# Performance work log

Hardware: AMD Instinct MI355X
Metric: run time of the kernel (lower is better)

Reference implementation:

```python
import jax, jax.numpy as jnp
import numpy as np

H = 1024      # hidden_size
NH = 16       # num_heads
DH = H // NH  # head dim
EPS = 1e-5

def layer_norm(x, g, b):
    m = jnp.mean(x, axis=-1, keepdims=True)
    v = jnp.mean(jnp.square(x - m), axis=-1, keepdims=True)
    return (x - m) * jax.lax.rsqrt(v + EPS) * g + b

def setup_inputs() -> dict:
    key = jax.random.key(0)
    ks = jax.random.split(key, 12)
    B, S = 4, 1024
    s = 0.02
    inp = {
        "x": jax.random.normal(ks[0], (B, S, H), jnp.float32),
        "attn_bias": jax.random.normal(ks[1], (B, NH, S, S), jnp.float32),
        # weights stored as (in, out): y = x @ W
        "W_Q": jax.random.normal(ks[2], (H, H), jnp.float32) * s,
        "W_K": jax.random.normal(ks[3], (H, H), jnp.float32) * s,
        "W_V": jax.random.normal(ks[4], (H, H), jnp.float32) * s,
        "W_O": jax.random.normal(ks[5], (H, H), jnp.float32) * s,
        "W_1": jax.random.normal(ks[6], (H, 4 * H), jnp.float32) * s,
        "W_2": jax.random.normal(ks[7], (H, 4 * H), jnp.float32) * s,
        "W_3": jax.random.normal(ks[8], (4 * H, H), jnp.float32) * s,
        "ln1_g": jnp.ones((H,), jnp.float32), "ln1_b": jnp.zeros((H,), jnp.float32),
        "ln2_g": jnp.ones((H,), jnp.float32), "ln2_b": jnp.zeros((H,), jnp.float32),
        "ln3_g": jnp.ones((H,), jnp.float32), "ln3_b": jnp.zeros((H,), jnp.float32),
        "ln4_g": jnp.ones((H,), jnp.float32), "ln4_b": jnp.zeros((H,), jnp.float32),
    }
    return inp

def reference(x, attn_bias, W_Q, W_K, W_V, W_O, W_1, W_2, W_3,
              ln1_g, ln1_b, ln2_g, ln2_b, ln3_g, ln3_b, ln4_g, ln4_b):
    B, S, _ = x.shape
    scale = DH ** -0.5
    # attn_in_norm
    xn = layer_norm(x, ln1_g, ln1_b)
    # biased multi-head attention
    Q = (xn @ W_Q).reshape(B, S, NH, DH)
    K = (xn @ W_K).reshape(B, S, NH, DH)
    V = (xn @ W_V).reshape(B, S, NH, DH)
    scores = jnp.einsum('bqhd,bkhd->bhqk', Q, K) * scale + attn_bias
    attn = jax.nn.softmax(scores, axis=-1)
    attn_out_prelinear = jnp.einsum('bhqk,bkhd->bqhd', attn, V).reshape(B, S, H)
    attn_out = layer_norm(attn_out_prelinear @ W_O, ln2_g, ln2_b)
    x_post_attn = x + attn_out  # dropout = identity (p=0 / eval)
    # bilinear FFN
    xn2 = layer_norm(x_post_attn, ln3_g, ln3_b)
    ff = ((xn2 @ W_1) * (xn2 @ W_2)) @ W_3
    ff_out = layer_norm(ff, ln4_g, ln4_b)
    x_post_ff = x_post_attn + ff_out
    return (x_post_attn, x_post_ff, attn_out_prelinear, ff_out)
```

## Files before the change

### kernel.cpp

```cpp
#include <hip/hip_runtime.h>
#include <math.h>

typedef unsigned short u16;
typedef unsigned int u32;
typedef __attribute__((ext_vector_type(8))) short short8v;
typedef __attribute__((ext_vector_type(4))) float f32x4;

#define H 1024
#define NH 16
#define DH 64
#define BB 4
#define SS 1024
#define MROWS (BB*SS)
#define FFD 4096
#define EPS 1e-5f
#define SCALE 0.125f

__device__ __forceinline__ u16 cvt_bf16(float v) {
  u32 u = __float_as_uint(v);
  return (u16)((u + 0x7fffu + ((u >> 16) & 1u)) >> 16);
}
__device__ __forceinline__ void split_bf16(float v, u16& h, u16& l) {
  u16 hh = cvt_bf16(v);
  float hf = __uint_as_float(((u32)hh) << 16);
  float r = v - hf;
  u16 ll = cvt_bf16(r);
  h = hh; l = ll;
}
__device__ __forceinline__ u32 pack2(u16 a, u16 b) { return (u32)a | ((u32)b << 16); }

#define GLL16(g, l) __builtin_amdgcn_global_load_lds( \
    (const __attribute__((address_space(1))) void*)(g), \
    (__attribute__((address_space(3))) void*)(l), 16, 0, 0)

#define VWAIT8 asm volatile("s_waitcnt vmcnt(8)" ::: "memory")
#define VWAIT6 asm volatile("s_waitcnt vmcnt(6)" ::: "memory")
#define VWAIT0 asm volatile("s_waitcnt vmcnt(0)" ::: "memory")
#define BAR_PRE  do { __builtin_amdgcn_s_barrier(); asm volatile("" ::: "memory"); } while (0)
#define BAR_POST do { asm volatile("" ::: "memory"); __builtin_amdgcn_s_barrier(); } while (0)

__global__ __launch_bounds__(256, 2) void gemm3_k(
    const u16* __restrict__ Ah, const u16* __restrict__ Al, int sA,
    const u16* __restrict__ B0h, const u16* __restrict__ B0l,
    const u16* __restrict__ B1h, const u16* __restrict__ B1l,
    const u16* __restrict__ B2h, const u16* __restrict__ B2l, int sB,
    float* C0, float* C1, float* C2,
    u16* E0h, u16* E0l, u16* E1h, u16* E1l, u16* EV,
    int sC, int K, int addC, int qkvmode)
{
  __shared__ u16 sAh0[4096], sAl0[4096], sBh0[4096], sBl0[4096];
  __shared__ u16 sAh1[4096], sAl1[4096], sBh1[4096], sBl1[4096];
  const int tid = threadIdx.x;
  const int wave = tid >> 6, lane = tid & 63;
  const int sel = blockIdx.x >> 3;
  const int bn = (blockIdx.x & 7) << 7;
  const int bm = blockIdx.y << 7;
  const u16* Bh = (sel == 0) ? B0h : (sel == 1) ? B1h : B2h;
  const u16* Bl = (sel == 0) ? B0l : (sel == 1) ? B1l : B2l;
  float* C = (sel == 0) ? C0 : (sel == 1) ? C1 : C2;

  const int c0 = wave, c1 = 4 + wave;
  const int row0 = c0 * 16 + (lane >> 2), row1 = c1 * 16 + (lane >> 2);
  const int sg0 = (lane & 3) ^ ((row0 >> 1) & 3);
  const int sg1 = (lane & 3) ^ ((row1 >> 1) & 3);
  const size_t offA0 = (size_t)(bm + row0) * sA + sg0 * 8;
  const size_t offA1 = (size_t)(bm + row1) * sA + sg1 * 8;
  const size_t offB0 = (size_t)(bn + row0) * sB + sg0 * 8;
  const size_t offB1 = (size_t)(bn + row1) * sB + sg1 * 8;

  const int kg = lane >> 4, r15 = lane & 15;
  const int wr = wave >> 1, wc = wave & 1;
  int aoff[4], boff[4];
  #pragma unroll
  for (int m = 0; m < 4; ++m) {
    int ra = wr * 64 + m * 16 + r15;
    aoff[m] = ra * 32 + ((kg ^ ((ra >> 1) & 3)) << 3);
    int rb = wc * 64 + m * 16 + r15;
    boff[m] = rb * 32 + ((kg ^ ((rb >> 1) & 3)) << 3);
  }

#define STAGE3(P, k0) do { \
    GLL16(Ah + offA0 + (k0), &sAh##P[c0 * 512]); \
    GLL16(Ah + offA1 + (k0), &sAh##P[c1 * 512]); \
    GLL16(Al + offA0 + (k0), &sAl##P[c0 * 512]); \
    GLL16(Al + offA1 + (k0), &sAl##P[c1 * 512]); \
    GLL16(Bh + offB0 + (k0), &sBh##P[c0 * 512]); \
    GLL16(Bh + offB1 + (k0), &sBh##P[c1 * 512]); \
    GLL16(Bl + offB0 + (k0), &sBl##P[c0 * 512]); \
    GLL16(Bl + offB1 + (k0), &sBl##P[c1 * 512]); \
  } while (0)

#define COMPUTE3(P) do { \
    short8v afh[4], afl[4], bfh[4], bfl[4]; \
    _Pragma("unroll") \
    for (int m = 0; m < 4; ++m) { \
      afh[m] = *(const short8v*)&sAh##P[aoff[m]]; \
      afl[m] = *(const short8v*)&sAl##P[aoff[m]]; \
      bfh[m] = *(const short8v*)&sBh##P[boff[m]]; \
      bfl[m] = *(const short8v*)&sBl##P[boff[m]]; \
    } \
    _Pragma("unroll") \
    for (int m = 0; m < 4; ++m) \
      _Pragma("unroll") \
      for (int n = 0; n < 4; ++n) { \
        acc[m][n] = __builtin_amdgcn_mfma_f32_16x16x32_bf16(afh[m], bfl[n], acc[m][n], 0, 0, 0); \
        acc[m][n] = __builtin_amdgcn_mfma_f32_16x16x32_bf16(afl[m], bfh[n], acc[m][n], 0, 0, 0); \
        acc[m][n] = __builtin_amdgcn_mfma_f32_16x16x32_bf16(afh[m], bfh[n], acc[m][n], 0, 0, 0); \
      } \
  } while (0)

  f32x4 acc[4][4] = {};
  STAGE3(0, 0);
  #pragma unroll 1
  for (int k0 = 0; k0 < K; k0 += 64) {
    if (k0 + 32 < K) { STAGE3(1, k0 + 32); VWAIT8; } else { VWAIT0; }
    BAR_PRE;
    COMPUTE3(0);
    BAR_POST;
    if (k0 + 64 < K) { STAGE3(0, k0 + 64); VWAIT8; } else { VWAIT0; }
    BAR_PRE;
    COMPUTE3(1);
    BAR_POST;
  }
#undef STAGE3
#undef COMPUTE3

  if (qkvmode) {
    #pragma unroll
    for (int m = 0; m < 4; ++m)
      #pragma unroll
      for (int n = 0; n < 4; ++n) {
        const int col = bn + wc * 64 + n * 16 + r15;
        const int rbase = bm + wr * 64 + m * 16 + (kg << 2);
        const int bhd = ((rbase >> 10) << 4) + (col >> 6);
        const int d = col & 63;
        const int seq0 = rbase & 1023;
        if (sel == 2) {
          ushort4 pk;
          pk.x = cvt_bf16(acc[m][n][0]); pk.y = cvt_bf16(acc[m][n][1]);
          pk.z = cvt_bf16(acc[m][n][2]); pk.w = cvt_bf16(acc[m][n][3]);
          *(ushort4*)&EV[((size_t)bhd * 64 + d) * SS + seq0] = pk;
        } else {
          u16* Th = (sel == 0) ? E0h : E1h;
          u16* Tl = (sel == 0) ? E0l : E1l;
          #pragma unroll
          for (int r = 0; r < 4; ++r) {
            u16 hh, ll; split_bf16(acc[m][n][r], hh, ll);
            const size_t idx = ((size_t)bhd * SS + seq0 + r) * DH + d;
            Th[idx] = hh; Tl[idx] = ll;
          }
        }
      }
  } else {
    #pragma unroll
    for (int m = 0; m < 4; ++m)
      #pragma unroll
      for (int n = 0; n < 4; ++n) {
        const int col = bn + wc * 64 + n * 16 + r15;
        #pragma unroll
        for (int r = 0; r < 4; ++r) {
          const int rr = bm + wr * 64 + m * 16 + (kg << 2) + r;
          const size_t idx = (size_t)rr * sC + col;
          float v = acc[m][n][r];
          if (addC) v += C[idx];
          C[idx] = v;
        }
      }
  }
}

__global__ __launch_bounds__(512, 1) void gemm_dual_k(
    const u16* __restrict__ Ah, const u16* __restrict__ Al, int sA,
    const u16* __restrict__ B1h, const u16* __restrict__ B1l,
    const u16* __restrict__ B2h, const u16* __restrict__ B2l, int sB,
    u16* __restrict__ Oh, u16* __restrict__ Ol, int sC, int K)
{
  __shared__ u16 sAh0[4096], sAl0[4096], s1h0[4096], s1l0[4096], s2h0[4096], s2l0[4096];
  __shared__ u16 sAh1[4096], sAl1[4096], s1h1[4096], s1l1[4096], s2h1[4096], s2l1[4096];
  const int tid = threadIdx.x;
  const int wave = tid >> 6, lane = tid & 63;
  const int bn = blockIdx.x << 7;
  const int bm = blockIdx.y << 7;

  const int srow = wave * 16 + (lane >> 2);
  const int sg = (lane & 3) ^ ((srow >> 1) & 3);
  const size_t offA = (size_t)(bm + srow) * sA + sg * 8;
  const size_t offB = (size_t)(bn + srow) * sB + sg * 8;

  const int kg = lane >> 4, r15 = lane & 15;
  const int wr = wave >> 2, wc = wave & 3;
  int aoff[4], boff[2];
  #pragma unroll
  for (int m = 0; m < 4; ++m) {
    int ra = wr * 64 + m * 16 + r15;
    aoff[m] = ra * 32 + ((kg ^ ((ra >> 1) & 3)) << 3);
  }
  #pragma unroll
  for (int n = 0; n < 2; ++n) {
    int rb = wc * 32 + n * 16 + r15;
    boff[n] = rb * 32 + ((kg ^ ((rb >> 1) & 3)) << 3);
  }

#define STAGED(P, k0) do { \
    GLL16(Ah  + offA + (k0), &sAh##P[wave * 512]); \
    GLL16(Al  + offA + (k0), &sAl##P[wave * 512]); \
    GLL16(B1h + offB + (k0), &s1h##P[wave * 512]); \
    GLL16(B1l + offB + (k0), &s1l##P[wave * 512]); \
    GLL16(B2h + offB + (k0), &s2h##P[wave * 512]); \
    GLL16(B2l + offB + (k0), &s2l##P[wave * 512]); \
  } while (0)

#define COMPUTED(P) do { \
    short8v afh[4], afl[4]; \
    _Pragma("unroll") \
    for (int m = 0; m < 4; ++m) { \
      afh[m] = *(const short8v*)&sAh##P[aoff[m]]; \
      afl[m] = *(const short8v*)&sAl##P[aoff[m]]; \
    } \
    _Pragma("unroll") \
    for (int n = 0; n < 2; ++n) { \
      short8v b1h = *(const short8v*)&s1h##P[boff[n]]; \
      short8v b1l = *(const short8v*)&s1l##P[boff[n]]; \
      short8v b2h = *(const short8v*)&s2h##P[boff[n]]; \
      short8v b2l = *(const short8v*)&s2l##P[boff[n]]; \
      _Pragma("unroll") \
      for (int m = 0; m < 4; ++m) { \
        acc1[m][n] = __builtin_amdgcn_mfma_f32_16x16x32_bf16(afh[m], b1l, acc1[m][n], 0, 0, 0); \
        acc1[m][n] = __builtin_amdgcn_mfma_f32_16x16x32_bf16(afl[m], b1h, acc1[m][n], 0, 0, 0); \
        acc1[m][n] = __builtin_amdgcn_mfma_f32_16x16x32_bf16(afh[m], b1h, acc1[m][n], 0, 0, 0); \
        acc2[m][n] = __builtin_amdgcn_mfma_f32_16x16x32_bf16(afh[m], b2l, acc2[m][n], 0, 0, 0); \
        acc2[m][n] = __builtin_amdgcn_mfma_f32_16x16x32_bf16(afl[m], b2h, acc2[m][n], 0, 0, 0); \
        acc2[m][n] = __builtin_amdgcn_mfma_f32_16x16x32_bf16(afh[m], b2h, acc2[m][n], 0, 0, 0); \
      } \
    } \
  } while (0)

  f32x4 acc1[4][2] = {}, acc2[4][2] = {};
  STAGED(0, 0);
  #pragma unroll 1
  for (int k0 = 0; k0 < K; k0 += 64) {
    if (k0 + 32 < K) { STAGED(1, k0 + 32); VWAIT6; } else { VWAIT0; }
    BAR_PRE;
    COMPUTED(0);
    BAR_POST;
    if (k0 + 64 < K) { STAGED(0, k0 + 64); VWAIT6; } else { VWAIT0; }
    BAR_PRE;
    COMPUTED(1);
    BAR_POST;
  }
#undef STAGED
#undef COMPUTED

  #pragma unroll
  for (int m = 0; m < 4; ++m)
    #pragma unroll
    for (int n = 0; n < 2; ++n) {
      const int col = bn + wc * 32 + n * 16 + r15;
      #pragma unroll
      for (int r = 0; r < 4; ++r) {
        const int rr = bm + wr * 64 + m * 16 + (kg << 2) + r;
        const size_t idx = (size_t)rr * sC + col;
        float p = acc1[m][n][r] * acc2[m][n][r];
        u16 hh, ll; split_bf16(p, hh, ll);
        Oh[idx] = hh; Ol[idx] = ll;
      }
    }
}

__global__ __launch_bounds__(256) void trsplit_k(const float* __restrict__ W,
    int R, int Cn, u16* __restrict__ Th, u16* __restrict__ Tl) {
  __shared__ float t[32][33];
  int n0 = blockIdx.x * 32, r0 = blockIdx.y * 32;
  int tx = threadIdx.x & 31, ty = threadIdx.x >> 5;
  #pragma unroll
  for (int i = 0; i < 4; ++i)
    t[ty + i * 8][tx] = W[(size_t)(r0 + ty + i * 8) * Cn + n0 + tx];
  __syncthreads();
  #pragma unroll
  for (int i = 0; i < 4; ++i) {
    float v = t[tx][ty + i * 8];
    u16 hh, ll; split_bf16(v, hh, ll);
    size_t o = (size_t)(n0 + ty + i * 8) * R + r0 + tx;
    Th[o] = hh; Tl[o] = ll;
  }
}

__global__ __launch_bounds__(256, 2) void attn_mfma_k(
    const u16* __restrict__ Qh, const u16* __restrict__ Ql,
    const u16* __restrict__ Kh, const u16* __restrict__ Kl,
    const u16* __restrict__ Vt, const float* __restrict__ bias,
    float* __restrict__ outp, u16* __restrict__ oph, u16* __restrict__ opl)
{
  __shared__ u16 sKh[4096], sKl[4096], sVt[4096];
  __shared__ u16 sP[5120];
  const int bh = blockIdx.y;
  const int q0 = blockIdx.x << 6;
  const int tid = threadIdx.x, w = tid >> 6, lane = tid & 63;
  const int kg = lane >> 4, r15 = lane & 15;

  short8v qfh[2], qfl[2];
  {
    const size_t qb = ((size_t)bh * SS + q0 + w * 16 + r15) * DH + kg * 8;
    qfh[0] = *(const short8v*)(Qh + qb);
    qfh[1] = *(const short8v*)(Qh + qb + 32);
    qfl[0] = *(const short8v*)(Ql + qb);
    qfl[1] = *(const short8v*)(Ql + qb + 32);
  }
  const int c0 = 2 * w, c1 = 2 * w + 1;
  const int sr0 = c0 * 8 + (lane >> 3), sr1 = c1 * 8 + (lane >> 3);
  const int sl0 = (lane & 7) ^ (sr0 & 7), sl1 = (lane & 7) ^ (sr1 & 7);
  const size_t kb0 = ((size_t)bh * SS + sr0) * DH + sl0 * 8;
  const size_t kb1 = ((size_t)bh * SS + sr1) * DH + sl1 * 8;
  const size_t vb0 = ((size_t)bh * DH + sr0) * SS + sl0 * 8;
  const size_t vb1 = ((size_t)bh * DH + sr1) * SS + sl1 * 8;
  const float* bp = bias + ((size_t)bh * SS + q0 + w * 16 + kg * 4) * SS + r15;

  float m_run[4], l_run[4];
  #pragma unroll
  for (int r = 0; r < 4; ++r) { m_run[r] = -1e30f; l_run[r] = 0.f; }
  f32x4 oacc[4] = {};

  #pragma unroll 1
  for (int t = 0; t < SS / 64; ++t) {
    const int k0 = t * 64;
    __syncthreads();
    GLL16(Kh + kb0 + (size_t)k0 * DH, &sKh[c0 * 512]);
    GLL16(Kh + kb1 + (size_t)k0 * DH, &sKh[c1 * 512]);
    GLL16(Kl + kb0 + (size_t)k0 * DH, &sKl[c0 * 512]);
    GLL16(Kl + kb1 + (size_t)k0 * DH, &sKl[c1 * 512]);
    GLL16(Vt + vb0 + k0, &sVt[c0 * 512]);
    GLL16(Vt + vb1 + k0, &sVt[c1 * 512]);
    float bv[4][4];
    #pragma unroll
    for (int r = 0; r < 4; ++r)
      #pragma unroll
      for (int nb = 0; nb < 4; ++nb)
        bv[r][nb] = bp[(size_t)r * SS + k0 + nb * 16];
    __syncthreads();

    f32x4 s[4] = {};
    #pragma unroll
    for (int nb = 0; nb < 4; ++nb) {
      const int krow = nb * 16 + r15;
      #pragma unroll
      for (int ks = 0; ks < 2; ++ks) {
        const int ch = (((ks * 4 + kg) ^ (krow & 7)) << 3);
        short8v kbh = *(const short8v*)&sKh[krow * 64 + ch];
        short8v kbl = *(const short8v*)&sKl[krow * 64 + ch];
        s[nb] = __builtin_amdgcn_mfma_f32_16x16x32_bf16(qfh[ks], kbl, s[nb], 0, 0, 0);
        s[nb] = __builtin_amdgcn_mfma_f32_16x16x32_bf16(qfl[ks], kbh, s[nb], 0, 0, 0);
        s[nb] = __builtin_amdgcn_mfma_f32_16x16x32_bf16(qfh[ks], kbh, s[nb], 0, 0, 0);
      }
    }
    float corr[4], p[4][4];
    #pragma unroll
    for (int r = 0; r < 4; ++r) {
      float a0 = fmaf(s[0][r], SCALE, bv[r][0]);
      float a1 = fmaf(s[1][r], SCALE, bv[r][1]);
      float a2 = fmaf(s[2][r], SCALE, bv[r][2]);
      float a3 = fmaf(s[3][r], SCALE, bv[r][3]);
      float m = fmaxf(fmaxf(a0, a1), fmaxf(a2, a3));
      m = fmaxf(m, __shfl_xor(m, 1));
      m = fmaxf(m, __shfl_xor(m, 2));
      m = fmaxf(m, __shfl_xor(m, 4));
      m = fmaxf(m, __shfl_xor(m, 8));
      const float mn = fmaxf(m_run[r], m);
      corr[r] = __expf(m_run[r] - mn);
      m_run[r] = mn;
      float e0 = __expf(a0 - mn), e1 = __expf(a1 - mn);
      float e2 = __expf(a2 - mn), e3 = __expf(a3 - mn);
      p[r][0] = e0; p[r][1] = e1; p[r][2] = e2; p[r][3] = e3;
      float l = e0 + e1 + e2 + e3;
      l += __shfl_xor(l, 1); l += __shfl_xor(l, 2);
      l += __shfl_xor(l, 4); l += __shfl_xor(l, 8);
      l_run[r] = l_run[r] * corr[r] + l;
    }
    #pragma unroll
    for (int r = 0; r < 4; ++r) {
      const int q = w * 16 + kg * 4 + r;
      #pragma unroll
      for (int nb = 0; nb < 4; ++nb) {
        const int col = nb * 16 + r15;
        sP[q * 80 + (((col >> 3) ^ (q & 7)) << 3) + (col & 7)] = cvt_bf16(p[r][nb]);
      }
    }
    #pragma unroll
    for (int nb = 0; nb < 4; ++nb) {
      oacc[nb][0] *= corr[0]; oacc[nb][1] *= corr[1];
      oacc[nb][2] *= corr[2]; oacc[nb][3] *= corr[3];
    }
    #pragma unroll
    for (int ks = 0; ks < 2; ++ks) {
      const int prow = w * 16 + r15;
      short8v pa = *(const short8v*)&sP[prow * 80 + (((ks * 4 + kg) ^ (r15 & 7)) << 3)];
      #pragma unroll
      for (int nb = 0; nb < 4; ++nb) {
        const int vrow = nb * 16 + r15;
        short8v vbv = *(const short8v*)&sVt[vrow * 64 + (((ks * 4 + kg) ^ (vrow & 7)) << 3)];
        oacc[nb] = __builtin_amdgcn_mfma_f32_16x16x32_bf16(pa, vbv, oacc[nb], 0, 0, 0);
      }
    }
  }
  const int b = bh >> 4, h = bh & 15;
  #pragma unroll
  for (int r = 0; r < 4; ++r) {
    const float inv = 1.0f / l_run[r];
    const int q = q0 + w * 16 + kg * 4 + r;
    const size_t base = ((size_t)(b * SS + q)) * H + h * 64 + r15;
    #pragma unroll
    for (int nb = 0; nb < 4; ++nb) {
      const float o = oacc[nb][r] * inv;
      outp[base + nb * 16] = o;
      u16 hh, ll; split_bf16(o, hh, ll);
      oph[base + nb * 16] = hh; opl[base + nb * 16] = ll;
    }
  }
}

__device__ __forceinline__ void blk_reduce2(float& s, float& s2, float* sh) {
  #pragma unroll
  for (int o = 32; o >= 1; o >>= 1) {
    s += __shfl_xor(s, o);
    s2 += __shfl_xor(s2, o);
  }
  int wid = threadIdx.x >> 6;
  if ((threadIdx.x & 63) == 0) { sh[wid] = s; sh[4 + wid] = s2; }
  __syncthreads();
  s = sh[0] + sh[1] + sh[2] + sh[3];
  s2 = sh[4] + sh[5] + sh[6] + sh[7];
}

__global__ __launch_bounds__(256) void ln1_k(const float* __restrict__ in,
    const float* __restrict__ g, const float* __restrict__ bb,
    u16* __restrict__ oh, u16* __restrict__ ol) {
  __shared__ float sh[8];
  int c = threadIdx.x << 2;
  size_t base = (size_t)blockIdx.x * H + c;
  float4 v = *(const float4*)(in + base);
  float s = v.x + v.y + v.z + v.w;
  float s2 = v.x * v.x + v.y * v.y + v.z * v.z + v.w * v.w;
  blk_reduce2(s, s2, sh);
  float mean = s * (1.f / H);
  float rstd = 1.f / sqrtf(s2 * (1.f / H) - mean * mean + EPS);
  float4 gv = *(const float4*)(g + c), bv = *(const float4*)(bb + c);
  float o0 = (v.x - mean) * rstd * gv.x + bv.x;
  float o1 = (v.y - mean) * rstd * gv.y + bv.y;
  float o2 = (v.z - mean) * rstd * gv.z + bv.z;
  float o3 = (v.w - mean) * rstd * gv.w + bv.w;
  u16 h0, l0, h1, l1, h2, l2, h3, l3;
  split_bf16(o0, h0, l0); split_bf16(o1, h1, l1);
  split_bf16(o2, h2, l2); split_bf16(o3, h3, l3);
  *(uint2*)(oh + base) = make_uint2(pack2(h0, h1), pack2(h2, h3));
  *(uint2*)(ol + base) = make_uint2(pack2(l0, l1), pack2(l2, l3));
}

__global__ __launch_bounds__(256) void ln2ln3_k(const float* __restrict__ oproj,
    const float* __restrict__ x, const float* __restrict__ g2, const float* __restrict__ b2,
    const float* __restrict__ g3, const float* __restrict__ b3,
    float* __restrict__ xpa_out, u16* __restrict__ xn2h, u16* __restrict__ xn2l) {
  __shared__ float shA[8], shB[8];
  int c = threadIdx.x << 2;
  size_t base = (size_t)blockIdx.x * H + c;
  float4 ov = *(const float4*)(oproj + base);
  float4 xv = *(const float4*)(x + base);
  float s = ov.x + ov.y + ov.z + ov.w;
  float s2 = ov.x * ov.x + ov.y * ov.y + ov.z * ov.z + ov.w * ov.w;
  blk_reduce2(s, s2, shA);
  float mean = s * (1.f / H);
  float rstd = 1.f / sqrtf(s2 * (1.f / H) - mean * mean + EPS);
  float4 g2v = *(const float4*)(g2 + c), b2v = *(const float4*)(b2 + c);
  float4 xpa;
  xpa.x = xv.x + (ov.x - mean) * rstd * g2v.x + b2v.x;
  xpa.y = xv.y + (ov.y - mean) * rstd * g2v.y + b2v.y;
  xpa.z = xv.z + (ov.z - mean) * rstd * g2v.z + b2v.z;
  xpa.w = xv.w + (ov.w - mean) * rstd * g2v.w + b2v.w;
  *(float4*)(xpa_out + base) = xpa;
  float t = xpa.x + xpa.y + xpa.z + xpa.w;
  float t2 = xpa.x * xpa.x + xpa.y * xpa.y + xpa.z * xpa.z + xpa.w * xpa.w;
  blk_reduce2(t, t2, shB);
  float mean3 = t * (1.f / H);
  float rstd3 = 1.f / sqrtf(t2 * (1.f / H) - mean3 * mean3 + EPS);
  float4 g3v = *(const float4*)(g3 + c), b3v = *(const float4*)(b3 + c);
  float o0 = (xpa.x - mean3) * rstd3 * g3v.x + b3v.x;
  float o1 = (xpa.y - mean3) * rstd3 * g3v.y + b3v.y;
  float o2 = (xpa.z - mean3) * rstd3 * g3v.z + b3v.z;
  float o3 = (xpa.w - mean3) * rstd3 * g3v.w + b3v.w;
  u16 h0, l0, h1, l1, h2, l2, h3, l3;
  split_bf16(o0, h0, l0); split_bf16(o1, h1, l1);
  split_bf16(o2, h2, l2); split_bf16(o3, h3, l3);
  *(uint2*)(xn2h + base) = make_uint2(pack2(h0, h1), pack2(h2, h3));
  *(uint2*)(xn2l + base) = make_uint2(pack2(l0, l1), pack2(l2, l3));
}

__global__ __launch_bounds__(256) void ln4_k(const float* ff,
    const float* __restrict__ xpa, const float* __restrict__ g4, const float* __restrict__ b4,
    float* ffout, float* __restrict__ xpf) {
  __shared__ float sh[8];
  int c = threadIdx.x << 2;
  size_t base = (size_t)blockIdx.x * H + c;
  float4 fv = *(const float4*)(ff + base);
  float s = fv.x + fv.y + fv.z + fv.w;
  float s2 = fv.x * fv.x + fv.y * fv.y + fv.z * fv.z + fv.w * fv.w;
  blk_reduce2(s, s2, sh);
  float mean = s * (1.f / H);
  float rstd = 1.f / sqrtf(s2 * (1.f / H) - mean * mean + EPS);
  float4 gv = *(const float4*)(g4 + c), bv = *(const float4*)(b4 + c);
  float4 fo;
  fo.x = (fv.x - mean) * rstd * gv.x + bv.x;
  fo.y = (fv.y - mean) * rstd * gv.y + bv.y;
  fo.z = (fv.z - mean) * rstd * gv.z + bv.z;
  fo.w = (fv.w - mean) * rstd * gv.w + bv.w;
  *(float4*)(ffout + base) = fo;
  float4 xv = *(const float4*)(xpa + base);
  *(float4*)(xpf + base) = make_float4(xv.x + fo.x, xv.y + fo.y, xv.z + fo.z, xv.w + fo.w);
}

extern "C" void kernel_launch(void* const* d_in, const int* in_sizes, int n_in,
                              void* d_out, int out_size, void* d_ws, size_t ws_size,
                              hipStream_t stream) {
  const float* x = (const float*)d_in[0];
  const float* bias = (const float*)d_in[1];
  const float* W_Q = (const float*)d_in[2];
  const float* W_K = (const float*)d_in[3];
  const float* W_V = (const float*)d_in[4];
  const float* W_O = (const float*)d_in[5];
  const float* W_1 = (const float*)d_in[6];
  const float* W_2 = (const float*)d_in[7];
  const float* W_3 = (const float*)d_in[8];
  const float* ln1g = (const float*)d_in[9];
  const float* ln1b = (const float*)d_in[10];
  const float* ln2g = (const float*)d_in[11];
  const float* ln2b = (const float*)d_in[12];
  const float* ln3g = (const float*)d_in[13];
  const float* ln3b = (const float*)d_in[14];
  const float* ln4g = (const float*)d_in[15];
  const float* ln4b = (const float*)d_in[16];

  float* out = (float*)d_out;
  const size_t T4 = (size_t)MROWS * H;
  float* xpa = out;
  float* xpf = out + T4;
  float* attnpre = out + 2 * T4;
  float* ffout = out + 3 * T4;

  char* ws = (char*)d_ws;
  const size_t MB = (size_t)1 << 20;
  u16* xn_h  = (u16*)(ws + 0 * MB);   u16* xn_l  = (u16*)(ws + 8 * MB);
  u16* WQt_h = (u16*)(ws + 16 * MB);  u16* WQt_l = (u16*)(ws + 18 * MB);
  u16* WKt_h = (u16*)(ws + 20 * MB);  u16* WKt_l = (u16*)(ws + 22 * MB);
  u16* WVt_h = (u16*)(ws + 24 * MB);  u16* WVt_l = (u16*)(ws + 26 * MB);
  u16* Qh = (u16*)(ws + 28 * MB);     u16* Ql = (u16*)(ws + 36 * MB);
  u16* Kh = (u16*)(ws + 44 * MB);     u16* Kl = (u16*)(ws + 52 * MB);
  u16* Vt = (u16*)(ws + 60 * MB);
  u16* ap_h = (u16*)(ws + 68 * MB);   u16* ap_l = (u16*)(ws + 76 * MB);
  u16* WOt_h = (u16*)(ws + 84 * MB);  u16* WOt_l = (u16*)(ws + 86 * MB);
  u16* xn2_h = (u16*)(ws + 88 * MB);  u16* xn2_l = (u16*)(ws + 96 * MB);
  u16* W1t_h = (u16*)(ws + 104 * MB); u16* W1t_l = (u16*)(ws + 112 * MB);
  u16* W2t_h = (u16*)(ws + 120 * MB); u16* W2t_l = (u16*)(ws + 128 * MB);
  u16* W3t_h = (u16*)(ws + 136 * MB); u16* W3t_l = (u16*)(ws + 144 * MB);
  u16* hb_h  = (u16*)(ws + 152 * MB); u16* hb_l  = (u16*)(ws + 184 * MB);
  float* oproj = xpf;
  float* ff = ffout;

  ln1_k<<<dim3(MROWS), dim3(256), 0, stream>>>(x, ln1g, ln1b, xn_h, xn_l);
  trsplit_k<<<dim3(32, 32), dim3(256), 0, stream>>>(W_Q, 1024, 1024, WQt_h, WQt_l);
  trsplit_k<<<dim3(32, 32), dim3(256), 0, stream>>>(W_K, 1024, 1024, WKt_h, WKt_l);
  trsplit_k<<<dim3(32, 32), dim3(256), 0, stream>>>(W_V, 1024, 1024, WVt_h, WVt_l);
  gemm3_k<<<dim3(24, 32), dim3(256), 0, stream>>>(xn_h, xn_l, 1024,
      WQt_h, WQt_l, WKt_h, WKt_l, WVt_h, WVt_l, 1024,
      nullptr, nullptr, nullptr,
      Qh, Ql, Kh, Kl, Vt, 1024, 1024, 0, 1);
  attn_mfma_k<<<dim3(16, 64), dim3(256), 0, stream>>>(Qh, Ql, Kh, Kl, Vt, bias,
      attnpre, ap_h, ap_l);
  trsplit_k<<<dim3(32, 32), dim3(256), 0, stream>>>(W_O, 1024, 1024, WOt_h, WOt_l);
  gemm3_k<<<dim3(8, 32), dim3(256), 0, stream>>>(ap_h, ap_l, 1024,
      WOt_h, WOt_l, WOt_h, WOt_l, WOt_h, WOt_l, 1024,
      oproj, oproj, oproj,
      nullptr, nullptr, nullptr, nullptr, nullptr, 1024, 1024, 0, 0);
  ln2ln3_k<<<dim3(MROWS), dim3(256), 0, stream>>>(oproj, x, ln2g, ln2b, ln3g, ln3b,
      xpa, xn2_h, xn2_l);
  trsplit_k<<<dim3(128, 32), dim3(256), 0, stream>>>(W_1, 1024, 4096, W1t_h, W1t_l);
  trsplit_k<<<dim3(128, 32), dim3(256), 0, stream>>>(W_2, 1024, 4096, W2t_h, W2t_l);
  trsplit_k<<<dim3(32, 128), dim3(256), 0, stream>>>(W_3, 4096, 1024, W3t_h, W3t_l);
  gemm_dual_k<<<dim3(32, 32), dim3(512), 0, stream>>>(xn2_h, xn2_l, 1024,
      W1t_h, W1t_l, W2t_h, W2t_l, 1024,
      hb_h, hb_l, 4096, 1024);
  gemm3_k<<<dim3(8, 32), dim3(256), 0, stream>>>(hb_h, hb_l, 4096,
      W3t_h, W3t_l, W3t_h, W3t_l, W3t_h, W3t_l, 4096,
      ff, ff, ff,
      nullptr, nullptr, nullptr, nullptr, nullptr, 1024, 4096, 0, 0);
  ln4_k<<<dim3(MROWS), dim3(256), 0, stream>>>(ff, xpa, ln4g, ln4b, ffout, xpf);
}
```

Before: 966.3 us.

## Split GEMM staging into half-steps with setprio, add 128x64 tile GEMM, batch transposes

Each GEMM k-step is split into two half-steps. Half the next tile's global-to-LDS loads are issued before each half's MFMAs, with finer vmcnt waits and s_setprio around the MFMA bursts, so loads overlap compute better. A new 128x64-tile GEMM kernel replaces the 128x128 kernel for the W_O and W_3 projections, doubling the grid from 256 to 512 blocks to fill more CUs. The weight transpose/split launches for Q/K/V and W1/W2 are merged into single z-batched kernels. The cost is extra barriers per k-step and more A-tile reloads from the smaller N tile.

```diff
diff --git a/kernel.cpp b/kernel.cpp
--- a/kernel.cpp
+++ b/kernel.cpp
@@ -33,11 +33,11 @@
     (const __attribute__((address_space(1))) void*)(g), \
     (__attribute__((address_space(3))) void*)(l), 16, 0, 0)
 
-#define VWAIT8 asm volatile("s_waitcnt vmcnt(8)" ::: "memory")
-#define VWAIT6 asm volatile("s_waitcnt vmcnt(6)" ::: "memory")
-#define VWAIT0 asm volatile("s_waitcnt vmcnt(0)" ::: "memory")
-#define BAR_PRE  do { __builtin_amdgcn_s_barrier(); asm volatile("" ::: "memory"); } while (0)
-#define BAR_POST do { asm volatile("" ::: "memory"); __builtin_amdgcn_s_barrier(); } while (0)
+#define VW4 asm volatile("s_waitcnt vmcnt(4)" ::: "memory")
+#define VW3 asm volatile("s_waitcnt vmcnt(3)" ::: "memory")
+#define VW0 asm volatile("s_waitcnt vmcnt(0)" ::: "memory")
+#define BARX do { asm volatile("" ::: "memory"); __builtin_amdgcn_s_barrier(); asm volatile("" ::: "memory"); } while (0)
+#define MFMA16(a, b, c) __builtin_amdgcn_mfma_f32_16x16x32_bf16((a), (b), (c), 0, 0, 0)
 
 __global__ __launch_bounds__(256, 2) void gemm3_k(
     const u16* __restrict__ Ah, const u16* __restrict__ Al, int sA,
@@ -79,51 +79,73 @@
     boff[m] = rb * 32 + ((kg ^ ((rb >> 1) & 3)) << 3);
   }
 
-#define STAGE3(P, k0) do { \
+#define STA3(P, k0) do { \
     GLL16(Ah + offA0 + (k0), &sAh##P[c0 * 512]); \
     GLL16(Ah + offA1 + (k0), &sAh##P[c1 * 512]); \
     GLL16(Al + offA0 + (k0), &sAl##P[c0 * 512]); \
     GLL16(Al + offA1 + (k0), &sAl##P[c1 * 512]); \
+  } while (0)
+#define STB3(P, k0) do { \
     GLL16(Bh + offB0 + (k0), &sBh##P[c0 * 512]); \
     GLL16(Bh + offB1 + (k0), &sBh##P[c1 * 512]); \
     GLL16(Bl + offB0 + (k0), &sBl##P[c0 * 512]); \
     GLL16(Bl + offB1 + (k0), &sBl##P[c1 * 512]); \
   } while (0)
 
-#define COMPUTE3(P) do { \
-    short8v afh[4], afl[4], bfh[4], bfl[4]; \
+#define SUBSTEP3(P, NXT, kn, hn) do { \
+    if (hn) { STA3(NXT, kn); VW4; } else { VW0; } \
+    BARX; \
+    short8v afh[4], afl[4], bfh[2], bfl[2]; \
     _Pragma("unroll") \
     for (int m = 0; m < 4; ++m) { \
       afh[m] = *(const short8v*)&sAh##P[aoff[m]]; \
       afl[m] = *(const short8v*)&sAl##P[aoff[m]]; \
-      bfh[m] = *(const short8v*)&sBh##P[boff[m]]; \
-      bfl[m] = *(const short8v*)&sBl##P[boff[m]]; \
-    } \
+    } \
+    _Pragma("unroll") \
+    for (int n = 0; n < 2; ++n) { \
+      bfh[n] = *(const short8v*)&sBh##P[boff[n]]; \
+      bfl[n] = *(const short8v*)&sBl##P[boff[n]]; \
+    } \
+    __builtin_amdgcn_s_setprio(1); \
     _Pragma("unroll") \
     for (int m = 0; m < 4; ++m) \
       _Pragma("unroll") \
-      for (int n = 0; n < 4; ++n) { \
-        acc[m][n] = __builtin_amdgcn_mfma_f32_16x16x32_bf16(afh[m], bfl[n], acc[m][n], 0, 0, 0); \
-        acc[m][n] = __builtin_amdgcn_mfma_f32_16x16x32_bf16(afl[m], bfh[n], acc[m][n], 0, 0, 0); \
-        acc[m][n] = __builtin_amdgcn_mfma_f32_16x16x32_bf16(afh[m], bfh[n], acc[m][n], 0, 0, 0); \
+      for (int n = 0; n < 2; ++n) { \
+        acc[m][n] = MFMA16(afh[m], bfl[n], acc[m][n]); \
+        acc[m][n] = MFMA16(afl[m], bfh[n], acc[m][n]); \
+        acc[m][n] = MFMA16(afh[m], bfh[n], acc[m][n]); \
       } \
+    __builtin_amdgcn_s_setprio(0); \
+    BARX; \
+    if (hn) { STB3(NXT, kn); } \
+    _Pragma("unroll") \
+    for (int n = 0; n < 2; ++n) { \
+      bfh[n] = *(const short8v*)&sBh##P[boff[2 + n]]; \
+      bfl[n] = *(const short8v*)&sBl##P[boff[2 + n]]; \
+    } \
+    __builtin_amdgcn_s_setprio(1); \
+    _Pragma("unroll") \
+    for (int m = 0; m < 4; ++m) \
+      _Pragma("unroll") \
+      for (int n = 0; n < 2; ++n) { \
+        acc[m][2 + n] = MFMA16(afh[m], bfl[n], acc[m][2 + n]); \
+        acc[m][2 + n] = MFMA16(afl[m], bfh[n], acc[m][2 + n]); \
+        acc[m][2 + n] = MFMA16(afh[m], bfh[n], acc[m][2 + n]); \
+      } \
+    __builtin_amdgcn_s_setprio(0); \
+    BARX; \
   } while (0)
 
   f32x4 acc[4][4] = {};
-  STAGE3(0, 0);
+  STA3(0, 0); STB3(0, 0);
   #pragma unroll 1
   for (int k0 = 0; k0 < K; k0 += 64) {
-    if (k0 + 32 < K) { STAGE3(1, k0 + 32); VWAIT8; } else { VWAIT0; }
-    BAR_PRE;
-    COMPUTE3(0);
-    BAR_POST;
-    if (k0 + 64 < K) { STAGE3(0, k0 + 64); VWAIT8; } else { VWAIT0; }
-    BAR_PRE;
-    COMPUTE3(1);
-    BAR_POST;
-  }
-#undef STAGE3
-#undef COMPUTE3
+    { const int kn = k0 + 32; const bool hn = kn < K; SUBSTEP3(0, 1, kn, hn); }
+    { const int kn = k0 + 64; const bool hn = kn < K; SUBSTEP3(1, 0, kn, hn); }
+  }
+#undef SUBSTEP3
+#undef STA3
+#undef STB3
 
   if (qkvmode) {
     #pragma unroll
@@ -169,6 +191,114 @@
   }
 }
 
+__global__ __launch_bounds__(256, 2) void gemm3n64_k(
+    const u16* __restrict__ Ah, const u16* __restrict__ Al, int sA,
+    const u16* __restrict__ Bh, const u16* __restrict__ Bl, int sB,
+    float* __restrict__ C, int sC, int K, int addC)
+{
+  __shared__ u16 sAh0[4096], sAl0[4096], sBh0[2048], sBl0[2048];
+  __shared__ u16 sAh1[4096], sAl1[4096], sBh1[2048], sBl1[2048];
+  const int tid = threadIdx.x;
+  const int wave = tid >> 6, lane = tid & 63;
+  const int bn = blockIdx.x << 6;
+  const int bm = blockIdx.y << 7;
+
+  const int c0 = wave, c1 = 4 + wave;
+  const int rowA0 = c0 * 16 + (lane >> 2), rowA1 = c1 * 16 + (lane >> 2);
+  const int sgA0 = (lane & 3) ^ ((rowA0 >> 1) & 3);
+  const int sgA1 = (lane & 3) ^ ((rowA1 >> 1) & 3);
+  const size_t offA0 = (size_t)(bm + rowA0) * sA + sgA0 * 8;
+  const size_t offA1 = (size_t)(bm + rowA1) * sA + sgA1 * 8;
+  const int rowB = wave * 16 + (lane >> 2);
+  const int sgB = (lane & 3) ^ ((rowB >> 1) & 3);
+  const size_t offB = (size_t)(bn + rowB) * sB + sgB * 8;
+
+  const int kg = lane >> 4, r15 = lane & 15;
+  const int wr = wave >> 1, wc = wave & 1;
+  int aoff[4], boff[2];
+  #pragma unroll
+  for (int m = 0; m < 4; ++m) {
+    int ra = wr * 64 + m * 16 + r15;
+    aoff[m] = ra * 32 + ((kg ^ ((ra >> 1) & 3)) << 3);
+  }
+  #pragma unroll
+  for (int n = 0; n < 2; ++n) {
+    int rb = wc * 32 + n * 16 + r15;
+    boff[n] = rb * 32 + ((kg ^ ((rb >> 1) & 3)) << 3);
+  }
+
+#define STN_H1(P, k0) do { \
+    GLL16(Ah + offA0 + (k0), &sAh##P[c0 * 512]); \
+    GLL16(Ah + offA1 + (k0), &sAh##P[c1 * 512]); \
+    GLL16(Al + offA0 + (k0), &sAl##P[c0 * 512]); \
+  } while (0)
+#define STN_H2(P, k0) do { \
+    GLL16(Al + offA1 + (k0), &sAl##P[c1 * 512]); \
+    GLL16(Bh + offB + (k0), &sBh##P[wave * 512]); \
+    GLL16(Bl + offB + (k0), &sBl##P[wave * 512]); \
+  } while (0)
+
+#define SUBSTEPN(P, NXT, kn, hn) do { \
+    if (hn) { STN_H1(NXT, kn); VW3; } else { VW0; } \
+    BARX; \
+    short8v afh[4], afl[4], bfh, bfl; \
+    _Pragma("unroll") \
+    for (int m = 0; m < 4; ++m) { \
+      afh[m] = *(const short8v*)&sAh##P[aoff[m]]; \
+      afl[m] = *(const short8v*)&sAl##P[aoff[m]]; \
+    } \
+    bfh = *(const short8v*)&sBh##P[boff[0]]; \
+    bfl = *(const short8v*)&sBl##P[boff[0]]; \
+    __builtin_amdgcn_s_setprio(1); \
+    _Pragma("unroll") \
+    for (int m = 0; m < 4; ++m) { \
+      acc[m][0] = MFMA16(afh[m], bfl, acc[m][0]); \
+      acc[m][0] = MFMA16(afl[m], bfh, acc[m][0]); \
+      acc[m][0] = MFMA16(afh[m], bfh, acc[m][0]); \
+    } \
+    __builtin_amdgcn_s_setprio(0); \
+    BARX; \
+    if (hn) { STN_H2(NXT, kn); } \
+    bfh = *(const short8v*)&sBh##P[boff[1]]; \
+    bfl = *(const short8v*)&sBl##P[boff[1]]; \
+    __builtin_amdgcn_s_setprio(1); \
+    _Pragma("unroll") \
+    for (int m = 0; m < 4; ++m) { \
+      acc[m][1] = MFMA16(afh[m], bfl, acc[m][1]); \
+      acc[m][1] = MFMA16(afl[m], bfh, acc[m][1]); \
+      acc[m][1] = MFMA16(afh[m], bfh, acc[m][1]); \
+    } \
+    __builtin_amdgcn_s_setprio(0); \
+    BARX; \
+  } while (0)
+
+  f32x4 acc[4][2] = {};
+  STN_H1(0, 0); STN_H2(0, 0);
+  #pragma unroll 1
+  for (int k0 = 0; k0 < K; k0 += 64) {
+    { const int kn = k0 + 32; const bool hn = kn < K; SUBSTEPN(0, 1, kn, hn); }
+    { const int kn = k0 + 64; const bool hn = kn < K; SUBSTEPN(1, 0, kn, hn); }
+  }
+#undef SUBSTEPN
+#undef STN_H1
+#undef STN_H2
+
+  #pragma unroll
+  for (int m = 0; m < 4; ++m)
+    #pragma unroll
+    for (int n = 0; n < 2; ++n) {
+      const int col = bn + wc * 32 + n * 16 + r15;
+      #pragma unroll
+      for (int r = 0; r < 4; ++r) {
+        const int rr = bm + wr * 64 + m * 16 + (kg << 2) + r;
+        const size_t idx = (size_t)rr * sC + col;
+        float v = acc[m][n][r];
+        if (addC) v += C[idx];
+        C[idx] = v;
+      }
+    }
+}
+
 __global__ __launch_bounds__(512, 1) void gemm_dual_k(
     const u16* __restrict__ Ah, const u16* __restrict__ Al, int sA,
     const u16* __restrict__ B1h, const u16* __restrict__ B1l,
@@ -201,17 +331,21 @@
     boff[n] = rb * 32 + ((kg ^ ((rb >> 1) & 3)) << 3);
   }
 
-#define STAGED(P, k0) do { \
+#define STD_H1(P, k0) do { \
     GLL16(Ah  + offA + (k0), &sAh##P[wave * 512]); \
     GLL16(Al  + offA + (k0), &sAl##P[wave * 512]); \
     GLL16(B1h + offB + (k0), &s1h##P[wave * 512]); \
+  } while (0)
+#define STD_H2(P, k0) do { \
     GLL16(B1l + offB + (k0), &s1l##P[wave * 512]); \
     GLL16(B2h + offB + (k0), &s2h##P[wave * 512]); \
     GLL16(B2l + offB + (k0), &s2l##P[wave * 512]); \
   } while (0)
 
-#define COMPUTED(P) do { \
-    short8v afh[4], afl[4]; \
+#define SUBSTEPD(P, NXT, kn, hn) do { \
+    if (hn) { STD_H1(NXT, kn); VW3; } else { VW0; } \
+    BARX; \
+    short8v afh[4], afl[4], bh[2], bl[2]; \
     _Pragma("unroll") \
     for (int m = 0; m < 4; ++m) { \
       afh[m] = *(const short8v*)&sAh##P[aoff[m]]; \
@@ -219,37 +353,49 @@
     } \
     _Pragma("unroll") \
     for (int n = 0; n < 2; ++n) { \
-      short8v b1h = *(const short8v*)&s1h##P[boff[n]]; \
-      short8v b1l = *(const short8v*)&s1l##P[boff[n]]; \
-      short8v b2h = *(const short8v*)&s2h##P[boff[n]]; \
-      short8v b2l = *(const short8v*)&s2l##P[boff[n]]; \
+      bh[n] = *(const short8v*)&s1h##P[boff[n]]; \
+      bl[n] = *(const short8v*)&s1l##P[boff[n]]; \
+    } \
+    __builtin_amdgcn_s_setprio(1); \
+    _Pragma("unroll") \
+    for (int n = 0; n < 2; ++n) \
       _Pragma("unroll") \
       for (int m = 0; m < 4; ++m) { \
-        acc1[m][n] = __builtin_amdgcn_mfma_f32_16x16x32_bf16(afh[m], b1l, acc1[m][n], 0, 0, 0); \
-        acc1[m][n] = __builtin_amdgcn_mfma_f32_16x16x32_bf16(afl[m], b1h, acc1[m][n], 0, 0, 0); \
-        acc1[m][n] = __builtin_amdgcn_mfma_f32_16x16x32_bf16(afh[m], b1h, acc1[m][n], 0, 0, 0); \
-        acc2[m][n] = __builtin_amdgcn_mfma_f32_16x16x32_bf16(afh[m], b2l, acc2[m][n], 0, 0, 0); \
-        acc2[m][n] = __builtin_amdgcn_mfma_f32_16x16x32_bf16(afl[m], b2h, acc2[m][n], 0, 0, 0); \
-        acc2[m][n] = __builtin_amdgcn_mfma_f32_16x16x32_bf16(afh[m], b2h, acc2[m][n], 0, 0, 0); \
+        acc1[m][n] = MFMA16(afh[m], bl[n], acc1[m][n]); \
+        acc1[m][n] = MFMA16(afl[m], bh[n], acc1[m][n]); \
+        acc1[m][n] = MFMA16(afh[m], bh[n], acc1[m][n]); \
       } \
-    } \
+    __builtin_amdgcn_s_setprio(0); \
+    BARX; \
+    if (hn) { STD_H2(NXT, kn); } \
+    _Pragma("unroll") \
+    for (int n = 0; n < 2; ++n) { \
+      bh[n] = *(const short8v*)&s2h##P[boff[n]]; \
+      bl[n] = *(const short8v*)&s2l##P[boff[n]]; \
+    } \
+    __builtin_amdgcn_s_setprio(1); \
+    _Pragma("unroll") \
+    for (int n = 0; n < 2; ++n) \
+      _Pragma("unroll") \
+      for (int m = 0; m < 4; ++m) { \
+        acc2[m][n] = MFMA16(afh[m], bl[n], acc2[m][n]); \
+        acc2[m][n] = MFMA16(afl[m], bh[n], acc2[m][n]); \
+        acc2[m][n] = MFMA16(afh[m], bh[n], acc2[m][n]); \
+      } \
+    __builtin_amdgcn_s_setprio(0); \
+    BARX; \
   } while (0)
 
   f32x4 acc1[4][2] = {}, acc2[4][2] = {};
-  STAGED(0, 0);
+  STD_H1(0, 0); STD_H2(0, 0);
   #pragma unroll 1
   for (int k0 = 0; k0 < K; k0 += 64) {
-    if (k0 + 32 < K) { STAGED(1, k0 + 32); VWAIT6; } else { VWAIT0; }
-    BAR_PRE;
-    COMPUTED(0);
-    BAR_POST;
-    if (k0 + 64 < K) { STAGED(0, k0 + 64); VWAIT6; } else { VWAIT0; }
-    BAR_PRE;
-    COMPUTED(1);
-    BAR_POST;
-  }
-#undef STAGED
-#undef COMPUTED
+    { const int kn = k0 + 32; const bool hn = kn < K; SUBSTEPD(0, 1, kn, hn); }
+    { const int kn = k0 + 64; const bool hn = kn < K; SUBSTEPD(1, 0, kn, hn); }
+  }
+#undef SUBSTEPD
+#undef STD_H1
+#undef STD_H2
 
   #pragma unroll
   for (int m = 0; m < 4; ++m)
@@ -270,6 +416,32 @@
 __global__ __launch_bounds__(256) void trsplit_k(const float* __restrict__ W,
     int R, int Cn, u16* __restrict__ Th, u16* __restrict__ Tl) {
   __shared__ float t[32][33];
+  int n0 = blockIdx.x * 32, r0 = blockIdx.y * 32;
+  int tx = threadIdx.x & 31, ty = threadIdx.x >> 5;
+  #pragma unroll
+  for (int i = 0; i < 4; ++i)
+    t[ty + i * 8][tx] = W[(size_t)(r0 + ty + i * 8) * Cn + n0 + tx];
+  __syncthreads();
+  #pragma unroll
+  for (int i = 0; i < 4; ++i) {
+    float v = t[tx][ty + i * 8];
+    u16 hh, ll; split_bf16(v, hh, ll);
+    size_t o = (size_t)(n0 + ty + i * 8) * R + r0 + tx;
+    Th[o] = hh; Tl[o] = ll;
+  }
+}
+
+__global__ __launch_bounds__(256) void trsplit3_k(
+    const float* __restrict__ W0, const float* __restrict__ W1, const float* __restrict__ W2,
+    int R, int Cn,
+    u16* __restrict__ T0h, u16* __restrict__ T0l,
+    u16* __restrict__ T1h, u16* __restrict__ T1l,
+    u16* __restrict__ T2h, u16* __restrict__ T2l) {
+  __shared__ float t[32][33];
+  const int z = blockIdx.z;
+  const float* W = (z == 0) ? W0 : (z == 1) ? W1 : W2;
+  u16* Th = (z == 0) ? T0h : (z == 1) ? T1h : T2h;
+  u16* Tl = (z == 0) ? T0l : (z == 1) ? T1l : T2l;
   int n0 = blockIdx.x * 32, r0 = blockIdx.y * 32;
   int tx = threadIdx.x & 31, ty = threadIdx.x >> 5;
   #pragma unroll
@@ -347,9 +519,9 @@
         const int ch = (((ks * 4 + kg) ^ (krow & 7)) << 3);
         short8v kbh = *(const short8v*)&sKh[krow * 64 + ch];
         short8v kbl = *(const short8v*)&sKl[krow * 64 + ch];
-        s[nb] = __builtin_amdgcn_mfma_f32_16x16x32_bf16(qfh[ks], kbl, s[nb], 0, 0, 0);
-        s[nb] = __builtin_amdgcn_mfma_f32_16x16x32_bf16(qfl[ks], kbh, s[nb], 0, 0, 0);
-        s[nb] = __builtin_amdgcn_mfma_f32_16x16x32_bf16(qfh[ks], kbh, s[nb], 0, 0, 0);
+        s[nb] = MFMA16(qfh[ks], kbl, s[nb]);
+        s[nb] = MFMA16(qfl[ks], kbh, s[nb]);
+        s[nb] = MFMA16(qfh[ks], kbh, s[nb]);
       }
     }
     float corr[4], p[4][4];
@@ -397,7 +569,7 @@
       for (int nb = 0; nb < 4; ++nb) {
         const int vrow = nb * 16 + r15;
         short8v vbv = *(const short8v*)&sVt[vrow * 64 + (((ks * 4 + kg) ^ (vrow & 7)) << 3)];
-        oacc[nb] = __builtin_amdgcn_mfma_f32_16x16x32_bf16(pa, vbv, oacc[nb], 0, 0, 0);
+        oacc[nb] = MFMA16(pa, vbv, oacc[nb]);
       }
     }
   }
@@ -563,9 +735,8 @@
   float* ff = ffout;
 
   ln1_k<<<dim3(MROWS), dim3(256), 0, stream>>>(x, ln1g, ln1b, xn_h, xn_l);
-  trsplit_k<<<dim3(32, 32), dim3(256), 0, stream>>>(W_Q, 1024, 1024, WQt_h, WQt_l);
-  trsplit_k<<<dim3(32, 32), dim3(256), 0, stream>>>(W_K, 1024, 1024, WKt_h, WKt_l);
-  trsplit_k<<<dim3(32, 32), dim3(256), 0, stream>>>(W_V, 1024, 1024, WVt_h, WVt_l);
+  trsplit3_k<<<dim3(32, 32, 3), dim3(256), 0, stream>>>(W_Q, W_K, W_V, 1024, 1024,
+      WQt_h, WQt_l, WKt_h, WKt_l, WVt_h, WVt_l);
   gemm3_k<<<dim3(24, 32), dim3(256), 0, stream>>>(xn_h, xn_l, 1024,
       WQt_h, WQt_l, WKt_h, WKt_l, WVt_h, WVt_l, 1024,
       nullptr, nullptr, nullptr,
@@ -573,21 +744,17 @@
   attn_mfma_k<<<dim3(16, 64), dim3(256), 0, stream>>>(Qh, Ql, Kh, Kl, Vt, bias,
       attnpre, ap_h, ap_l);
   trsplit_k<<<dim3(32, 32), dim3(256), 0, stream>>>(W_O, 1024, 1024, WOt_h, WOt_l);
-  gemm3_k<<<dim3(8, 32), dim3(256), 0, stream>>>(ap_h, ap_l, 1024,
-      WOt_h, WOt_l, WOt_h, WOt_l, WOt_h, WOt_l, 1024,
-      oproj, oproj, oproj,
-      nullptr, nullptr, nullptr, nullptr, nullptr, 1024, 1024, 0, 0);
+  gemm3n64_k<<<dim3(16, 32), dim3(256), 0, stream>>>(ap_h, ap_l, 1024,
+      WOt_h, WOt_l, 1024, oproj, 1024, 1024, 0);
   ln2ln3_k<<<dim3(MROWS), dim3(256), 0, stream>>>(oproj, x, ln2g, ln2b, ln3g, ln3b,
       xpa, xn2_h, xn2_l);
-  trsplit_k<<<dim3(128, 32), dim3(256), 0, stream>>>(W_1, 1024, 4096, W1t_h, W1t_l);
-  trsplit_k<<<dim3(128, 32), dim3(256), 0, stream>>>(W_2, 1024, 4096, W2t_h, W2t_l);
+  trsplit3_k<<<dim3(128, 32, 2), dim3(256), 0, stream>>>(W_1, W_2, W_2, 1024, 4096,
+      W1t_h, W1t_l, W2t_h, W2t_l, W2t_h, W2t_l);
   trsplit_k<<<dim3(32, 128), dim3(256), 0, stream>>>(W_3, 4096, 1024, W3t_h, W3t_l);
   gemm_dual_k<<<dim3(32, 32), dim3(512), 0, stream>>>(xn2_h, xn2_l, 1024,
       W1t_h, W1t_l, W2t_h, W2t_l, 1024,
       hb_h, hb_l, 4096, 1024);
-  gemm3_k<<<dim3(8, 32), dim3(256), 0, stream>>>(hb_h, hb_l, 4096,
-      W3t_h, W3t_l, W3t_h, W3t_l, W3t_h, W3t_l, 4096,
-      ff, ff, ff,
-      nullptr, nullptr, nullptr, nullptr, nullptr, 1024, 4096, 0, 0);
+  gemm3n64_k<<<dim3(16, 32), dim3(256), 0, stream>>>(hb_h, hb_l, 4096,
+      W3t_h, W3t_l, 4096, ff, 1024, 4096, 0);
   ln4_k<<<dim3(MROWS), dim3(256), 0, stream>>>(ff, xpa, ln4g, ln4b, ffout, xpf);
 }
```

New measurement: 977.2 us. About the same (+1.1%).
